# Optimization experiments

Measured on AMD Instinct MI355X. Metric: run time of the kernel, lower is better.

## Reference

```python
import jax, jax.numpy as jnp
import numpy as np

EPS = 1e-7  # K.epsilon()
ATTN_WIDTH = 12
B, L, D = 8, 4096, 768


def setup_inputs() -> dict:
    key = jax.random.key(0)
    k1, k2 = jax.random.split(key)
    x = jax.random.normal(k1, (B, L, D), dtype=jnp.float32)
    Wa = jax.random.normal(k2, (D, 1), dtype=jnp.float32) * 0.05  # RandomNormal(stddev=0.05)
    return {"x": x, "Wa": Wa}


def reference(x, Wa):
    """Banded rank-1 self-attention.

    e[b,i,j] = u[b,i]*u[b,j] with u = x @ Wa, masked to the trailing band
    i-w+1 <= j <= i, normalized by the row sum (+eps), then v = a @ x.
    Because e is rank-1 inside the band, we never materialize the LxL matrix:
      wsum_i  = sum_{j=i-w+1}^{i} u_j          (windowed cumsum)
      wvec_i  = sum_{j=i-w+1}^{i} u_j * x_j    (windowed cumsum of u*x)
      v_i     = u_i * wvec_i / (u_i * wsum_i + eps)
    which is exactly e/(sum(e)+eps) @ x.
    """
    w = ATTN_WIDTH
    u = jnp.einsum('bld,do->bl', x, Wa)            # [B, L]
    cu = jnp.cumsum(u, axis=1)                      # [B, L]
    cux = jnp.cumsum(u[..., None] * x, axis=1)      # [B, L, D]
    # shifted[i] = cu[i-w] (0 for i < w)
    cu_shift = jnp.pad(cu, ((0, 0), (w, 0)))[:, :L]
    cux_shift = jnp.pad(cux, ((0, 0), (w, 0), (0, 0)))[:, :L, :]
    wsum = cu - cu_shift                            # [B, L]
    wvec = cux - cux_shift                          # [B, L, D]
    denom = u * wsum + EPS                          # [B, L]
    v = (u[..., None] * wvec) / denom[..., None]    # [B, L, D]
    return v
```

## Files before the change

### kernel.cpp

```cpp
#include <hip/hip_runtime.h>

typedef float vfloat4 __attribute__((ext_vector_type(4)));

namespace {
constexpr int kB = 8;
constexpr int kL = 4096;
constexpr int kD = 768;
constexpr int kW = 12;
constexpr int kHalo = kW - 1;
constexpr float kEps = 1e-7f;

constexpr int kRowsPerBlockU = 16;
constexpr int kGridU = kB * kL / kRowsPerBlockU;

constexpr int kT2 = 16;
constexpr int kRows2 = kT2 + kHalo;
constexpr int kThreads2 = 192;
constexpr int kChunks2 = kL / kT2;
constexpr int kGridV = kB * kChunks2;
}

__global__ __launch_bounds__(256, 4) void compute_u_kernel(
    const float* __restrict__ x, const float* __restrict__ Wa,
    double* __restrict__ u) {
  const int lane = threadIdx.x & 63;
  const int wv = threadIdx.x >> 6;
  const int rg0 = blockIdx.x * kRowsPerBlockU + wv * 4;

  vfloat4 w[3];
#pragma unroll
  for (int k = 0; k < 3; ++k)
    w[k] = *(const vfloat4*)(Wa + 4 * lane + 256 * k);

  vfloat4 xv[4][3];
#pragma unroll
  for (int q = 0; q < 4; ++q)
#pragma unroll
    for (int k = 0; k < 3; ++k)
      xv[q][k] = *(const vfloat4*)(x + (size_t)(rg0 + q) * kD + 4 * lane + 256 * k);

  double acc[4];
#pragma unroll
  for (int q = 0; q < 4; ++q) {
    double p = 0.0;
#pragma unroll
    for (int k = 0; k < 3; ++k) {
      p += (double)xv[q][k].x * (double)w[k].x + (double)xv[q][k].y * (double)w[k].y +
           (double)xv[q][k].z * (double)w[k].z + (double)xv[q][k].w * (double)w[k].w;
    }
    acc[q] = p;
  }
#pragma unroll
  for (int q = 0; q < 4; ++q) {
#pragma unroll
    for (int s = 32; s >= 1; s >>= 1) acc[q] += __shfl_xor(acc[q], s, 64);
  }
  if (lane == 0) {
#pragma unroll
    for (int q = 0; q < 4; ++q) u[rg0 + q] = acc[q];
  }
}

__global__ __launch_bounds__(kThreads2, 3) void banded_v_kernel(
    const float* __restrict__ x, const double* __restrict__ u,
    float* __restrict__ out) {
  __shared__ float s_uf[kRows2];
  __shared__ float s_scale[kT2];

  const int blk = blockIdx.x;
  const int b = blk / kChunks2;
  const int i0 = (blk % kChunks2) * kT2;
  const float* xb = x + (size_t)b * kL * kD;
  float* ob = out + (size_t)b * kL * kD;
  const double* ub = u + (size_t)b * kL;
  const int tid = threadIdx.x;

  if (tid < kRows2) {
    const int row = i0 - kHalo + tid;
    s_uf[tid] = (row >= 0) ? (float)ub[row] : 0.0f;
  } else if (tid >= 64 && tid < 64 + kT2) {
    const int t = tid - 64;
    const int i = i0 + t;
    double wsum = 0.0;
#pragma unroll
    for (int k = 0; k < kW; ++k) {
      const int j = i - kHalo + k;
      if (j >= 0) wsum += ub[j];
    }
    const double uu = ub[i];
    s_scale[t] = (float)(uu / (uu * wsum + (double)kEps));
  }
  __syncthreads();

  float uf[kRows2];
#pragma unroll
  for (int r = 0; r < kRows2; ++r) uf[r] = s_uf[r];
  float sc[kT2];
#pragma unroll
  for (int t = 0; t < kT2; ++t) sc[t] = s_scale[t];

  const int c0 = 4 * tid;
  vfloat4 ring[kW];
#pragma unroll
  for (int r = 0; r < kHalo; ++r) {
    const int row = i0 - kHalo + r;
    vfloat4 v = {0.f, 0.f, 0.f, 0.f};
    if (row >= 0) v = *(const vfloat4*)(xb + (size_t)row * kD + c0);
    ring[r] = v;
  }

#pragma unroll
  for (int t = 0; t < kT2; ++t) {
    const int i = i0 + t;
    const int r = kHalo + t;
    ring[r % kW] = *(const vfloat4*)(xb + (size_t)i * kD + c0);
    vfloat4 acc = {0.f, 0.f, 0.f, 0.f};
#pragma unroll
    for (int j = 0; j < kW; ++j) {
      const float uu = uf[r - j];
      const vfloat4 xv = ring[(r - j) % kW];
      acc.x += uu * xv.x; acc.y += uu * xv.y;
      acc.z += uu * xv.z; acc.w += uu * xv.w;
    }
    const float s = sc[t];
    vfloat4 o = {s * acc.x, s * acc.y, s * acc.z, s * acc.w};
    __builtin_nontemporal_store(o, (vfloat4*)(ob + (size_t)i * kD + c0));
  }
}

extern "C" void kernel_launch(void* const* d_in, const int* in_sizes, int n_in,
                              void* d_out, int out_size, void* d_ws, size_t ws_size,
                              hipStream_t stream) {
  const float* x = (const float*)d_in[0];
  const float* Wa = (const float*)d_in[1];
  float* out = (float*)d_out;
  double* u = (double*)d_ws;

  compute_u_kernel<<<kGridU, 256, 0, stream>>>(x, Wa, u);
  banded_v_kernel<<<kGridV, kThreads2, 0, stream>>>(x, u, out);
}
```

Before: 198.7 us.

## Fuse projection and banded attention into a single kernel with halo recompute

Merges the u-projection kernel into the banded attention kernel. Each block computes u for its 16 rows plus the 11-row halo directly into shared memory, then derives the window sums and scales locally. This removes a separate full pass over x, the global u workspace, and one kernel launch. In exchange it recomputes halo dot products redundantly and adds register pressure from holding 27 vectors and doing double-precision reductions.

```diff
diff --git a/kernel.cpp b/kernel.cpp
--- a/kernel.cpp
+++ b/kernel.cpp
@@ -10,94 +10,105 @@
 constexpr int kHalo = kW - 1;
 constexpr float kEps = 1e-7f;
 
-constexpr int kRowsPerBlockU = 16;
-constexpr int kGridU = kB * kL / kRowsPerBlockU;
-
-constexpr int kT2 = 16;
-constexpr int kRows2 = kT2 + kHalo;
-constexpr int kThreads2 = 192;
-constexpr int kChunks2 = kL / kT2;
-constexpr int kGridV = kB * kChunks2;
+constexpr int kT = 16;
+constexpr int kRows = kT + kHalo;
+constexpr int kThreads = 192;
+constexpr int kChunks = kL / kT;
+constexpr int kGrid = kB * kChunks;
 }
 
-__global__ __launch_bounds__(256, 4) void compute_u_kernel(
+__global__ __launch_bounds__(kThreads, 3) void fused_banded_kernel(
     const float* __restrict__ x, const float* __restrict__ Wa,
-    double* __restrict__ u) {
-  const int lane = threadIdx.x & 63;
-  const int wv = threadIdx.x >> 6;
-  const int rg0 = blockIdx.x * kRowsPerBlockU + wv * 4;
+    float* __restrict__ out) {
+  __shared__ double s_ud[kRows];
+  __shared__ float s_uf[kRows];
+  __shared__ float s_scale[kT];
+
+  const int blk = blockIdx.x;
+  const int b = blk / kChunks;
+  const int i0 = (blk % kChunks) * kT;
+  const float* xb = x + (size_t)b * kL * kD;
+  float* ob = out + (size_t)b * kL * kD;
+  const int tid = threadIdx.x;
+  const int lane = tid & 63;
+  const int wv = tid >> 6;
 
   vfloat4 w[3];
 #pragma unroll
   for (int k = 0; k < 3; ++k)
     w[k] = *(const vfloat4*)(Wa + 4 * lane + 256 * k);
 
-  vfloat4 xv[4][3];
+  if (i0 >= kHalo) {
+    vfloat4 xv[9][3];
 #pragma unroll
-  for (int q = 0; q < 4; ++q)
+    for (int it = 0; it < 9; ++it) {
+      const int row = i0 - kHalo + wv + 3 * it;
 #pragma unroll
-    for (int k = 0; k < 3; ++k)
-      xv[q][k] = *(const vfloat4*)(x + (size_t)(rg0 + q) * kD + 4 * lane + 256 * k);
-
-  double acc[4];
+      for (int k = 0; k < 3; ++k)
+        xv[it][k] = *(const vfloat4*)(xb + (size_t)row * kD + 4 * lane + 256 * k);
+    }
+    double p[9];
 #pragma unroll
-  for (int q = 0; q < 4; ++q) {
-    double p = 0.0;
+    for (int it = 0; it < 9; ++it) {
+      double q = 0.0;
 #pragma unroll
-    for (int k = 0; k < 3; ++k) {
-      p += (double)xv[q][k].x * (double)w[k].x + (double)xv[q][k].y * (double)w[k].y +
-           (double)xv[q][k].z * (double)w[k].z + (double)xv[q][k].w * (double)w[k].w;
+      for (int k = 0; k < 3; ++k) {
+        q += (double)xv[it][k].x * (double)w[k].x + (double)xv[it][k].y * (double)w[k].y +
+             (double)xv[it][k].z * (double)w[k].z + (double)xv[it][k].w * (double)w[k].w;
+      }
+      p[it] = q;
     }
-    acc[q] = p;
-  }
 #pragma unroll
-  for (int q = 0; q < 4; ++q) {
+    for (int s = 32; s >= 1; s >>= 1) {
 #pragma unroll
-    for (int s = 32; s >= 1; s >>= 1) acc[q] += __shfl_xor(acc[q], s, 64);
-  }
-  if (lane == 0) {
+      for (int it = 0; it < 9; ++it) p[it] += __shfl_xor(p[it], s, 64);
+    }
+    if (lane == 0) {
 #pragma unroll
-    for (int q = 0; q < 4; ++q) u[rg0 + q] = acc[q];
-  }
-}
-
-__global__ __launch_bounds__(kThreads2, 3) void banded_v_kernel(
-    const float* __restrict__ x, const double* __restrict__ u,
-    float* __restrict__ out) {
-  __shared__ float s_uf[kRows2];
-  __shared__ float s_scale[kT2];
-
-  const int blk = blockIdx.x;
-  const int b = blk / kChunks2;
-  const int i0 = (blk % kChunks2) * kT2;
-  const float* xb = x + (size_t)b * kL * kD;
-  float* ob = out + (size_t)b * kL * kD;
-  const double* ub = u + (size_t)b * kL;
-  const int tid = threadIdx.x;
-
-  if (tid < kRows2) {
-    const int row = i0 - kHalo + tid;
-    s_uf[tid] = (row >= 0) ? (float)ub[row] : 0.0f;
-  } else if (tid >= 64 && tid < 64 + kT2) {
-    const int t = tid - 64;
-    const int i = i0 + t;
-    double wsum = 0.0;
+      for (int it = 0; it < 9; ++it) {
+        const int lr = wv + 3 * it;
+        s_ud[lr] = p[it];
+        s_uf[lr] = (float)p[it];
+      }
+    }
+  } else {
 #pragma unroll
-    for (int k = 0; k < kW; ++k) {
-      const int j = i - kHalo + k;
-      if (j >= 0) wsum += ub[j];
+    for (int it = 0; it < 9; ++it) {
+      const int lr = wv + 3 * it;
+      const int row = i0 - kHalo + lr;
+      double p = 0.0;
+      if (row >= 0) {
+        vfloat4 xv[3];
+#pragma unroll
+        for (int k = 0; k < 3; ++k)
+          xv[k] = *(const vfloat4*)(xb + (size_t)row * kD + 4 * lane + 256 * k);
+#pragma unroll
+        for (int k = 0; k < 3; ++k) {
+          p += (double)xv[k].x * (double)w[k].x + (double)xv[k].y * (double)w[k].y +
+               (double)xv[k].z * (double)w[k].z + (double)xv[k].w * (double)w[k].w;
+        }
+#pragma unroll
+        for (int s = 32; s >= 1; s >>= 1) p += __shfl_xor(p, s, 64);
+      }
+      if (lane == 0) {
+        s_ud[lr] = p;
+        s_uf[lr] = (float)p;
+      }
     }
-    const double uu = ub[i];
-    s_scale[t] = (float)(uu / (uu * wsum + (double)kEps));
   }
   __syncthreads();
 
-  float uf[kRows2];
+  float uf[kRows];
 #pragma unroll
-  for (int r = 0; r < kRows2; ++r) uf[r] = s_uf[r];
-  float sc[kT2];
+  for (int r = 0; r < kRows; ++r) uf[r] = s_uf[r];
+
+  if (tid < kT) {
+    double wsum = 0.0;
 #pragma unroll
-  for (int t = 0; t < kT2; ++t) sc[t] = s_scale[t];
+    for (int k = 0; k < kW; ++k) wsum += s_ud[tid + k];
+    const double uu = s_ud[tid + kHalo];
+    s_scale[tid] = (float)(uu / (uu * wsum + (double)kEps));
+  }
 
   const int c0 = 4 * tid;
   vfloat4 ring[kW];
@@ -108,9 +119,14 @@
     if (row >= 0) v = *(const vfloat4*)(xb + (size_t)row * kD + c0);
     ring[r] = v;
   }
+  __syncthreads();
+
+  float sc[kT];
+#pragma unroll
+  for (int t = 0; t < kT; ++t) sc[t] = s_scale[t];
 
 #pragma unroll
-  for (int t = 0; t < kT2; ++t) {
+  for (int t = 0; t < kT; ++t) {
     const int i = i0 + t;
     const int r = kHalo + t;
     ring[r % kW] = *(const vfloat4*)(xb + (size_t)i * kD + c0);
@@ -134,8 +150,7 @@
   const float* x = (const float*)d_in[0];
   const float* Wa = (const float*)d_in[1];
   float* out = (float*)d_out;
-  double* u = (double*)d_ws;
+  (void)d_ws; (void)ws_size;
 
-  compute_u_kernel<<<kGridU, 256, 0, stream>>>(x, Wa, u);
-  banded_v_kernel<<<kGridV, kThreads2, 0, stream>>>(x, u, out);
+  fused_banded_kernel<<<kGrid, kThreads, 0, stream>>>(x, Wa, out);
 }
```

Measured after the change: 198.7 us. No clear change (-0.0%).

## Halve banded tile, drop LDS sync, issue all x/u loads upfront per thread

Applied to the files above, without the earlier changes.

The tile of output rows per block drops from 16 to 8, and the shared-memory staging plus __syncthreads is removed. Each thread now loads all halo and tile rows of x and u directly into registers before computing, and the per-row scales are computed redundantly per lane and broadcast with width-8 shuffles. The goal is to expose more memory-level parallelism and remove the barrier stall. The cost is a larger halo fraction: 19 rows are read for every 8 written instead of 27 for 16, which adds redundant x traffic and more blocks.

```diff
diff --git a/kernel.cpp b/kernel.cpp
--- a/kernel.cpp
+++ b/kernel.cpp
@@ -13,8 +13,8 @@
 constexpr int kRowsPerBlockU = 16;
 constexpr int kGridU = kB * kL / kRowsPerBlockU;
 
-constexpr int kT2 = 16;
-constexpr int kRows2 = kT2 + kHalo;
+constexpr int kT2 = 8;
+constexpr int kRing = kT2 + kHalo;
 constexpr int kThreads2 = 192;
 constexpr int kChunks2 = kL / kT2;
 constexpr int kGridV = kB * kChunks2;
@@ -64,9 +64,6 @@
 __global__ __launch_bounds__(kThreads2, 3) void banded_v_kernel(
     const float* __restrict__ x, const double* __restrict__ u,
     float* __restrict__ out) {
-  __shared__ float s_uf[kRows2];
-  __shared__ float s_scale[kT2];
-
   const int blk = blockIdx.x;
   const int b = blk / kChunks2;
   const int i0 = (blk % kChunks2) * kT2;
@@ -74,57 +71,63 @@
   float* ob = out + (size_t)b * kL * kD;
   const double* ub = u + (size_t)b * kL;
   const int tid = threadIdx.x;
+  const int lane = tid & 63;
+  const int c0 = 4 * tid;
 
-  if (tid < kRows2) {
-    const int row = i0 - kHalo + tid;
-    s_uf[tid] = (row >= 0) ? (float)ub[row] : 0.0f;
-  } else if (tid >= 64 && tid < 64 + kT2) {
-    const int t = tid - 64;
-    const int i = i0 + t;
+  vfloat4 xr[kRing];
+  float ufr[kRing];
+  if (i0 >= kHalo) {
+#pragma unroll
+    for (int r = 0; r < kRing; ++r)
+      xr[r] = *(const vfloat4*)(xb + (size_t)(i0 - kHalo + r) * kD + c0);
+#pragma unroll
+    for (int r = 0; r < kRing; ++r)
+      ufr[r] = (float)ub[i0 - kHalo + r];
+  } else {
+#pragma unroll
+    for (int r = 0; r < kRing; ++r) {
+      const int row = i0 - kHalo + r;
+      vfloat4 v = {0.f, 0.f, 0.f, 0.f};
+      float uu = 0.0f;
+      if (row >= 0) {
+        v = *(const vfloat4*)(xb + (size_t)row * kD + c0);
+        uu = (float)ub[row];
+      }
+      xr[r] = v;
+      ufr[r] = uu;
+    }
+  }
+
+  {
+    const int myt = lane & 7;
+    const int il = i0 + myt;
     double wsum = 0.0;
 #pragma unroll
     for (int k = 0; k < kW; ++k) {
-      const int j = i - kHalo + k;
+      const int j = il - kHalo + k;
       if (j >= 0) wsum += ub[j];
     }
-    const double uu = ub[i];
-    s_scale[t] = (float)(uu / (uu * wsum + (double)kEps));
-  }
-  __syncthreads();
-
-  float uf[kRows2];
+    const double uu = ub[il];
+    const float msc = (float)(uu / (uu * wsum + (double)kEps));
+    float sc[kT2];
 #pragma unroll
-  for (int r = 0; r < kRows2; ++r) uf[r] = s_uf[r];
-  float sc[kT2];
-#pragma unroll
-  for (int t = 0; t < kT2; ++t) sc[t] = s_scale[t];
-
-  const int c0 = 4 * tid;
-  vfloat4 ring[kW];
-#pragma unroll
-  for (int r = 0; r < kHalo; ++r) {
-    const int row = i0 - kHalo + r;
-    vfloat4 v = {0.f, 0.f, 0.f, 0.f};
-    if (row >= 0) v = *(const vfloat4*)(xb + (size_t)row * kD + c0);
-    ring[r] = v;
-  }
+    for (int t = 0; t < kT2; ++t) sc[t] = __shfl(msc, t, 8);
 
 #pragma unroll
-  for (int t = 0; t < kT2; ++t) {
-    const int i = i0 + t;
-    const int r = kHalo + t;
-    ring[r % kW] = *(const vfloat4*)(xb + (size_t)i * kD + c0);
-    vfloat4 acc = {0.f, 0.f, 0.f, 0.f};
+    for (int t = 0; t < kT2; ++t) {
+      vfloat4 acc = {0.f, 0.f, 0.f, 0.f};
 #pragma unroll
-    for (int j = 0; j < kW; ++j) {
-      const float uu = uf[r - j];
-      const vfloat4 xv = ring[(r - j) % kW];
-      acc.x += uu * xv.x; acc.y += uu * xv.y;
-      acc.z += uu * xv.z; acc.w += uu * xv.w;
+      for (int j = 0; j < kW; ++j) {
+        const int r = kHalo + t - j;
+        const float uu2 = ufr[r];
+        const vfloat4 xv = xr[r];
+        acc.x += uu2 * xv.x; acc.y += uu2 * xv.y;
+        acc.z += uu2 * xv.z; acc.w += uu2 * xv.w;
+      }
+      const float s = sc[t];
+      vfloat4 o = {s * acc.x, s * acc.y, s * acc.z, s * acc.w};
+      __builtin_nontemporal_store(o, (vfloat4*)(ob + (size_t)(i0 + t) * kD + c0));
     }
-    const float s = sc[t];
-    vfloat4 o = {s * acc.x, s * acc.y, s * acc.z, s * acc.w};
-    __builtin_nontemporal_store(o, (vfloat4*)(ob + (size_t)i * kD + c0));
   }
 }
 
@@ -135,6 +138,7 @@
   const float* Wa = (const float*)d_in[1];
   float* out = (float*)d_out;
   double* u = (double*)d_ws;
+  (void)ws_size;
 
   compute_u_kernel<<<kGridU, 256, 0, stream>>>(x, Wa, u);
   banded_v_kernel<<<kGridV, kThreads2, 0, stream>>>(x, u, out);
```

New measurement: 213.7 us. 7.5% more time.
